# Kernel tuning notes

Hardware: AMD Instinct MI355X
Metric: run time of the kernel (lower is better)

The kernel has to match this reference:

```python
import jax, jax.numpy as jnp
import numpy as np

ALPHA = 0.2  # LeakyReLU negative slope


def setup_inputs() -> dict:
    key = jax.random.key(0)
    k1, k2, k3, k4 = jax.random.split(key, 4)
    B, Cin, Cout, N, T, Kt = 8, 64, 64, 2048, 13, 3
    L = T - Kt + 1  # 11, must equal `length`
    x = jax.random.normal(k1, (B, Cin, N, T), dtype=jnp.float32)
    w0 = jax.random.normal(k2, (Cout, Cin, 1, Kt), dtype=jnp.float32) * 0.05
    b0 = jax.random.normal(k3, (Cout,), dtype=jnp.float32) * 0.05
    w1 = jax.random.normal(k4, (Cout * L,), dtype=jnp.float32) * 0.05
    return {"x": x, "w0": w0, "b0": b0, "w1": w1}


def reference(x, w0, b0, w1):
    # conv0: Conv2d(in,out,(1,Kt)), VALID padding -> [B, Cout, N, L]
    h = jax.lax.conv_general_dilated(
        x, w0, window_strides=(1, 1), padding='VALID',
        dimension_numbers=('NCHW', 'OIHW', 'NCHW')) + b0[None, :, None, None]
    B, C, N, L = h.shape
    # permute(0,1,3,2).view(B, C*L, N) then 1x1 Conv1d (no bias) == contraction over (c,l)
    # NOTE: original module uses conv1 for BOTH f_1 and f_2 (conv2 unused), so f_1 == f_2.
    f = jnp.einsum('bcnl,cl->bn', h, w1.reshape(C, L))  # [B, N]
    logits = f[:, :, None] + f[:, None, :]              # [B, N, N]
    lrelu = jnp.where(logits >= 0, logits, ALPHA * logits)
    attention = jax.nn.softmax(lrelu, axis=-1)          # softmax over last (column) dim
    attention = jnp.swapaxes(attention, -1, -2)         # [B, N, N] transposed
    # h_prime[b,c,q,l] = sum_n h[b,c,n,l] * attention[b,n,q]
    h_prime = jnp.einsum('bcnl,bnq->bcql', h, attention)
    return h_prime, attention
```

## Files before the change

### kernel.cpp

```cpp
#include <hip/hip_runtime.h>

#define BB 8
#define CIN 64
#define COUT 64
#define NN 2048
#define TT 13
#define KTT 3
#define LL 11
#define CL 704
#define HP_SIZE 11534336LL

#define BM 176
#define BN 128
#define A_TILE 5632

#define WS_TAB_OFF 65568ULL
#define WS_W0PK_OFF 327712ULL
#define WS_APAN_OFF 352288ULL

typedef _Float16 f16;
typedef __attribute__((ext_vector_type(8))) _Float16 f16x8;
typedef __attribute__((ext_vector_type(2))) _Float16 f16x2;
typedef __attribute__((ext_vector_type(4))) float f32x4;

__device__ __forceinline__ unsigned int pk16(float a, float b) {
  f16 ha = (f16)a, hb = (f16)b;
  unsigned short ua = __builtin_bit_cast(unsigned short, ha);
  unsigned short ub = __builtin_bit_cast(unsigned short, hb);
  return (unsigned int)ua | ((unsigned int)ub << 16);
}
__device__ __forceinline__ f16x2 as_h2(unsigned int u) {
  return __builtin_bit_cast(f16x2, u);
}

__global__ __launch_bounds__(256) void k_pack(const float* __restrict__ w0,
                                              unsigned int* __restrict__ w0pk_g) {
  int tid = blockIdx.x * 256 + threadIdx.x;
  int c = tid & 63, r = tid >> 6;
  int kt = r % 3, cip = r / 3;
  float ev = w0[c * 192 + cip * 6 + kt];
  float od = w0[c * 192 + cip * 6 + 3 + kt];
  w0pk_g[r * 64 + c] = pk16(ev, od);
}

__global__ __launch_bounds__(512, 4) void k_conv(
    const float* __restrict__ x, const unsigned int* __restrict__ w0pk_g,
    const float* __restrict__ b0, const float* __restrict__ w1,
    f16* __restrict__ Apan, float* __restrict__ f) {
  __shared__ unsigned int w0pk[96 * 64];
  __shared__ unsigned int xspk[32 * 8 * 16];
  __shared__ f16 As[704 * 10];
  const int tid = threadIdx.x;
  const int b = blockIdx.x >> 8;
  const int n0 = (blockIdx.x & 255) << 3;

#pragma unroll
  for (int i = 0; i < 12; ++i) w0pk[i * 512 + tid] = w0pk_g[i * 512 + tid];

#pragma unroll
  for (int i = 0; i < 7; ++i) {
    int task = i * 512 + tid;
    if (task < 3328) {
      int cip = task / 104, rem = task - cip * 104;
      long long base = (long long)(b * 64 + 2 * cip) * 26624 + n0 * 13 + rem;
      float ev = x[base];
      float od = x[base + 26624];
      int n = rem / 13, t = rem - n * 13;
      xspk[(cip * 8 + n) * 16 + t] = pk16(ev, od);
    }
  }
  __syncthreads();

  const int c = tid & 63, w = tid >> 6;
  float acc[11];
  const float bias = b0[c];
#pragma unroll
  for (int l = 0; l < 11; ++l) acc[l] = bias;

  for (int cip = 0; cip < 32; ++cip) {
    const unsigned int* xr = &xspk[(cip * 8 + w) * 16];
    uint4 xa = *(const uint4*)xr;
    uint4 xb = *(const uint4*)(xr + 4);
    uint4 xc = *(const uint4*)(xr + 8);
    unsigned int x13[13] = {xa.x, xa.y, xa.z, xa.w, xb.x, xb.y, xb.z, xb.w,
                            xc.x, xc.y, xc.z, xc.w, xr[12]};
    f16x2 wk0 = as_h2(w0pk[(cip * 3 + 0) * 64 + c]);
    f16x2 wk1 = as_h2(w0pk[(cip * 3 + 1) * 64 + c]);
    f16x2 wk2 = as_h2(w0pk[(cip * 3 + 2) * 64 + c]);
#pragma unroll
    for (int l = 0; l < 11; ++l) {
      acc[l] = __builtin_amdgcn_fdot2(as_h2(x13[l]), wk0, acc[l], false);
      acc[l] = __builtin_amdgcn_fdot2(as_h2(x13[l + 1]), wk1, acc[l], false);
      acc[l] = __builtin_amdgcn_fdot2(as_h2(x13[l + 2]), wk2, acc[l], false);
    }
  }

  float p = 0.f;
#pragma unroll
  for (int l = 0; l < 11; ++l) p = fmaf(acc[l], w1[c * 11 + l], p);
#pragma unroll
  for (int off = 32; off; off >>= 1) p += __shfl_xor(p, off, 64);
  if (c == 0) f[b * 2048 + n0 + w] = p;

#pragma unroll
  for (int l = 0; l < 11; ++l) As[(c * 11 + l) * 10 + w] = (f16)acc[l];
  __syncthreads();

  const int ks = n0 >> 5, kc4 = (n0 >> 3) & 3;
  const unsigned int* As32 = (const unsigned int*)As;
#pragma unroll
  for (int i = 0; i < 2; ++i) {
    int m = i * 512 + tid;
    if (m < 704) {
      uint4 v;
      v.x = As32[m * 5 + 0];
      v.y = As32[m * 5 + 1];
      v.z = As32[m * 5 + 2];
      v.w = As32[m * 5 + 3];
      int ct = m / 176, mo = m - ct * 176;
      long long base = ((long long)(b * 4 + ct) * 64 + ks) * A_TILE + kc4 * 1408 + mo * 8;
      *(uint4*)&Apan[base] = v;
    }
  }
}

__global__ __launch_bounds__(256) void k_maxf(const float* __restrict__ f,
                                              float* __restrict__ maxf) {
  const int b = blockIdx.x, tid = threadIdx.x;
  float m = -1e30f;
  for (int i = tid; i < 2048; i += 256) m = fmaxf(m, f[b * 2048 + i]);
#pragma unroll
  for (int off = 32; off; off >>= 1) m = fmaxf(m, __shfl_xor(m, off, 64));
  __shared__ float red[4];
  if ((tid & 63) == 0) red[tid >> 6] = m;
  __syncthreads();
  if (tid == 0) maxf[b] = fmaxf(fmaxf(red[0], red[1]), fmaxf(red[2], red[3]));
}

__global__ __launch_bounds__(256) void k_rowsum(const float* __restrict__ f,
                                                const float* __restrict__ maxf,
                                                float4* __restrict__ tab4) {
  __shared__ float fs[2048];
  const int b = blockIdx.x >> 9;
  const int q0 = (blockIdx.x & 511) << 2;
  const int tid = threadIdx.x;
#pragma unroll
  for (int i = 0; i < 8; ++i) fs[i * 256 + tid] = f[b * 2048 + i * 256 + tid];
  __syncthreads();
  const int lane = tid & 63, wid = tid >> 6;
  const int q = q0 + wid;
  const float fq = fs[q];
  const float mb = maxf[b];
  float t = fq + mb;
  const float m = t >= 0.f ? t : 0.2f * t;
  float sum = 0.f;
  for (int j = lane; j < 2048; j += 64) {
    float v = fq + fs[j];
    v = v >= 0.f ? v : 0.2f * v;
    sum += __expf(v - m);
  }
#pragma unroll
  for (int off = 32; off; off >>= 1) sum += __shfl_xor(sum, off, 64);
  if (lane == 0) {
    float rq = 1.0f / sum;
    float En = __expf(fq - mb);
    float E2 = __expf(0.2f * fq);
    float Rq = t >= 0.f ? rq : rq * __expf(0.8f * t);
    float Sq = rq * __expf(0.2f * fq - m);
    tab4[b * 2048 + q] = make_float4(En, E2, Rq, Sq);
  }
}

__global__ __launch_bounds__(256, 2) void k_gemm(const f16* __restrict__ Apan,
                                                 const float* __restrict__ f,
                                                 const float4* __restrict__ tab4,
                                                 float* __restrict__ att,
                                                 float* __restrict__ out) {
  __shared__ __align__(16) f16 Abuf[2][A_TILE];
  __shared__ __align__(16) f16 Bbuf[2][4096];
  __shared__ float fs[2048];
  __shared__ __align__(16) float2 Etab[2048];

  const int p = blockIdx.x;
  const int g = (p & 7) | ((p >> 7) << 3);
  const int qt = (p >> 3) & 15;
  const int ct = g & 3, b = g >> 2;

  const int tid = threadIdx.x;
  const int w = tid >> 6, lane = tid & 63, qp = lane & 15, gg = lane >> 4;
  const int wq = w * 32;
  const f16* Ab = Apan + (long long)(b * 4 + ct) * 64 * A_TILE;
  const float* fb = f + b * NN;
  const float4* tb = tab4 + (long long)b * NN;

#pragma unroll
  for (int i = 0; i < 2; ++i)
    ((float4*)fs)[i * 256 + tid] = ((const float4*)fb)[i * 256 + tid];
#pragma unroll
  for (int i = 0; i < 8; ++i) {
    float4 v = tb[i * 256 + tid];
    Etab[i * 256 + tid] = make_float2(v.x, v.y);
  }

  const int qb = tid & 127, kh = tid >> 7;
  const float fq = fb[qt * 128 + qb];
  const float4 myt = tb[qt * 128 + qb];
  const float Rq = myt.z, Sq = myt.w;

  f32x4 acc[11][2];
#pragma unroll
  for (int mf = 0; mf < 11; ++mf)
#pragma unroll
    for (int nf = 0; nf < 2; ++nf) acc[mf][nf] = (f32x4){0.f, 0.f, 0.f, 0.f};

  auto stageA = [&](int ks, int bsel) {
    const f16* a = Ab + (long long)ks * A_TILE;
    f16* l = Abuf[bsel];
#pragma unroll
    for (int i = 0; i < 3; ++i) {
      int ch = i * 4 + w;
      if (ch < 11)
        __builtin_amdgcn_global_load_lds(
            (const __attribute__((address_space(1))) unsigned int*)(a + ch * 512 + lane * 8),
            (__attribute__((address_space(3))) unsigned int*)(l + ch * 512), 16, 0, 0);
    }
  };
  auto buildB = [&](int ks, int bsel) {
    f16* Bs = Bbuf[bsel];
    const int nbase = ks * 32 + kh * 16;
#pragma unroll
    for (int h8 = 0; h8 < 2; ++h8) {
      float4 fA = *(const float4*)&fs[nbase + h8 * 8];
      float4 fB = *(const float4*)&fs[nbase + h8 * 8 + 4];
      const float4* ep = (const float4*)&Etab[nbase + h8 * 8];
      float4 e0 = ep[0], e1 = ep[1], e2 = ep[2], e3 = ep[3];
      float fn[8] = {fA.x, fA.y, fA.z, fA.w, fB.x, fB.y, fB.z, fB.w};
      float Ev[8] = {e0.x, e0.z, e1.x, e1.z, e2.x, e2.z, e3.x, e3.z};
      float E2v[8] = {e0.y, e0.w, e1.y, e1.w, e2.y, e2.w, e3.y, e3.w};
      f16x8 v8;
      float vf[8];
#pragma unroll
      for (int u = 0; u < 8; ++u) {
        bool pos = (fq + fn[u]) >= 0.f;
        float val = (pos ? Ev[u] : E2v[u]) * (pos ? Rq : Sq);
        vf[u] = val;
        v8[u] = (f16)val;
      }
      *(f16x8*)&Bs[((kh * 2 + h8) * 128 + qb) * 8] = v8;
      if ((ks >> 4) == ct) {
        long long nb = (long long)(b * 2048 + nbase + h8 * 8) * 2048 + qt * 128 + qb;
#pragma unroll
        for (int u = 0; u < 8; ++u) att[nb + (long long)u * 2048] = vf[u];
      }
    }
  };
  auto compute = [&](int bsel) {
    const f16* A = Abuf[bsel];
    const f16* Bt = Bbuf[bsel];
    f16x8 bh[2];
#pragma unroll
    for (int nf = 0; nf < 2; ++nf)
      bh[nf] = *(const f16x8*)&Bt[(gg * 128 + wq + nf * 16 + qp) * 8];
#pragma unroll
    for (int mf = 0; mf < 11; ++mf) {
      f16x8 av = *(const f16x8*)&A[(gg * 176 + mf * 16 + qp) * 8];
#pragma unroll
      for (int nf = 0; nf < 2; ++nf)
        acc[mf][nf] = __builtin_amdgcn_mfma_f32_16x16x32_f16(av, bh[nf], acc[mf][nf], 0, 0, 0);
    }
  };

  stageA(0, 0);
  __syncthreads();
  buildB(0, 0);
  __syncthreads();

  int cur = 0;
  for (int ks = 0; ks < 63; ++ks) {
    stageA(ks + 1, cur ^ 1);
    buildB(ks + 1, cur ^ 1);
    compute(cur);
    __syncthreads();
    cur ^= 1;
  }
  compute(cur);

  float* ob = out + (long long)b * COUT * NN * LL;
#pragma unroll
  for (int mf = 0; mf < 11; ++mf) {
#pragma unroll
    for (int r = 0; r < 4; ++r) {
      int m = ct * BM + mf * 16 + gg * 4 + r;
      int c = m / 11, l2 = m - c * 11;
      float* orow = ob + (long long)c * NN * LL + l2;
#pragma unroll
      for (int nf = 0; nf < 2; ++nf) {
        int q = qt * BN + wq + nf * 16 + qp;
        orow[(long long)q * LL] = acc[mf][nf][r];
      }
    }
  }
}

extern "C" void kernel_launch(void* const* d_in, const int* in_sizes, int n_in,
                              void* d_out, int out_size, void* d_ws, size_t ws_size,
                              hipStream_t stream) {
  const float* x  = (const float*)d_in[0];
  const float* w0 = (const float*)d_in[1];
  const float* b0 = (const float*)d_in[2];
  const float* w1 = (const float*)d_in[3];

  float* fbuf = (float*)d_ws;
  float* maxf = fbuf + BB * NN;
  float4* tab4 = (float4*)((char*)d_ws + WS_TAB_OFF);
  unsigned int* w0pk_g = (unsigned int*)((char*)d_ws + WS_W0PK_OFF);
  f16* Apan = (f16*)((char*)d_ws + WS_APAN_OFF);

  float* hp  = (float*)d_out;
  float* att = hp + HP_SIZE;

  k_pack<<<dim3(24), dim3(256), 0, stream>>>(w0, w0pk_g);
  k_conv<<<dim3(BB * 256), dim3(512), 0, stream>>>(x, w0pk_g, b0, w1, Apan, fbuf);
  k_maxf<<<dim3(BB), dim3(256), 0, stream>>>(fbuf, maxf);
  k_rowsum<<<dim3(BB * 512), dim3(256), 0, stream>>>(fbuf, maxf, tab4);
  k_gemm<<<dim3(512), dim3(256), 0, stream>>>(Apan, fbuf, tab4, att, hp);
}
```

Baseline: 161.3 us.

## Split attention write into separate kernel and widen GEMM tile to 256 columns

Moves the fp32 attention-matrix store out of the GEMM's B-tile builder into a dedicated k_att kernel that writes rows with coalesced float4 stores, where before it was a strided per-element store. The GEMM now uses 512-thread blocks with a 176x256 tile, so each block builds B for twice as many columns and covers the 11 M-fragments with two wave groups. This removes the uncoalesced global writes from the GEMM's inner loop and halves the grid. In exchange it adds a launch, recomputes the attention values a second time, and leaves the second wave group with uneven fragment work.

```diff
diff --git a/kernel.cpp b/kernel.cpp
--- a/kernel.cpp
+++ b/kernel.cpp
@@ -11,7 +11,7 @@
 #define HP_SIZE 11534336LL
 
 #define BM 176
-#define BN 128
+#define BN 256
 #define A_TILE 5632
 
 #define WS_TAB_OFF 65568ULL
@@ -31,6 +31,11 @@
 }
 __device__ __forceinline__ f16x2 as_h2(unsigned int u) {
   return __builtin_bit_cast(f16x2, u);
+}
+__device__ __forceinline__ void gl_lds16(const f16* g, f16* l) {
+  __builtin_amdgcn_global_load_lds(
+      (const __attribute__((address_space(1))) unsigned int*)g,
+      (__attribute__((address_space(3))) unsigned int*)l, 16, 0, 0);
 }
 
 __global__ __launch_bounds__(256) void k_pack(const float* __restrict__ w0,
@@ -171,58 +176,95 @@
   }
 }
 
-__global__ __launch_bounds__(256, 2) void k_gemm(const f16* __restrict__ Apan,
+__global__ __launch_bounds__(256) void k_att(const float* __restrict__ f,
+                                             const float4* __restrict__ tab4,
+                                             float* __restrict__ att) {
+  const int b = blockIdx.x >> 9;
+  const int i0 = (blockIdx.x & 511) << 2;
+  const int tid = threadIdx.x;
+  const float* fb = f + b * NN;
+  const float4* tb = tab4 + (long long)b * NN;
+
+  float fi[4], En[4], E2[4];
+#pragma unroll
+  for (int r = 0; r < 4; ++r) {
+    fi[r] = fb[i0 + r];
+    float4 t = tb[i0 + r];
+    En[r] = t.x;
+    E2[r] = t.y;
+  }
+  const int j0 = tid * 8;
+  float4 fj0 = *(const float4*)&fb[j0];
+  float4 fj1 = *(const float4*)&fb[j0 + 4];
+  float fj[8] = {fj0.x, fj0.y, fj0.z, fj0.w, fj1.x, fj1.y, fj1.z, fj1.w};
+  float Rq[8], Sq[8];
+#pragma unroll
+  for (int u = 0; u < 8; ++u) {
+    float4 t = tb[j0 + u];
+    Rq[u] = t.z;
+    Sq[u] = t.w;
+  }
+  float* ab = att + ((long long)(b * 2048 + i0)) * 2048 + j0;
+#pragma unroll
+  for (int r = 0; r < 4; ++r) {
+    float o[8];
+#pragma unroll
+    for (int u = 0; u < 8; ++u) {
+      bool pos = (fi[r] + fj[u]) >= 0.f;
+      o[u] = (pos ? En[r] : E2[r]) * (pos ? Rq[u] : Sq[u]);
+    }
+    float* orow = ab + (long long)r * 2048;
+    *(float4*)&orow[0] = make_float4(o[0], o[1], o[2], o[3]);
+    *(float4*)&orow[4] = make_float4(o[4], o[5], o[6], o[7]);
+  }
+}
+
+__global__ __launch_bounds__(512, 2) void k_gemm(const f16* __restrict__ Apan,
                                                  const float* __restrict__ f,
                                                  const float4* __restrict__ tab4,
-                                                 float* __restrict__ att,
                                                  float* __restrict__ out) {
   __shared__ __align__(16) f16 Abuf[2][A_TILE];
-  __shared__ __align__(16) f16 Bbuf[2][4096];
+  __shared__ __align__(16) f16 Bbuf[2][8192];
   __shared__ float fs[2048];
   __shared__ __align__(16) float2 Etab[2048];
 
   const int p = blockIdx.x;
-  const int g = (p & 7) | ((p >> 7) << 3);
-  const int qt = (p >> 3) & 15;
+  const int g = (p & 7) | ((p >> 6) << 3);
+  const int qt = (p >> 3) & 7;
   const int ct = g & 3, b = g >> 2;
 
   const int tid = threadIdx.x;
   const int w = tid >> 6, lane = tid & 63, qp = lane & 15, gg = lane >> 4;
-  const int wq = w * 32;
+  const int qw = w & 3, mw = w >> 2;
   const f16* Ab = Apan + (long long)(b * 4 + ct) * 64 * A_TILE;
   const float* fb = f + b * NN;
   const float4* tb = tab4 + (long long)b * NN;
 
-#pragma unroll
-  for (int i = 0; i < 2; ++i)
-    ((float4*)fs)[i * 256 + tid] = ((const float4*)fb)[i * 256 + tid];
-#pragma unroll
-  for (int i = 0; i < 8; ++i) {
-    float4 v = tb[i * 256 + tid];
-    Etab[i * 256 + tid] = make_float2(v.x, v.y);
-  }
-
-  const int qb = tid & 127, kh = tid >> 7;
-  const float fq = fb[qt * 128 + qb];
-  const float4 myt = tb[qt * 128 + qb];
+  ((float4*)fs)[tid] = ((const float4*)fb)[tid];
+#pragma unroll
+  for (int i = 0; i < 4; ++i) {
+    float4 v = tb[i * 512 + tid];
+    Etab[i * 512 + tid] = make_float2(v.x, v.y);
+  }
+
+  const int qb = tid & 255, kh = tid >> 8;
+  const float fq = fb[qt * 256 + qb];
+  const float4 myt = tb[qt * 256 + qb];
   const float Rq = myt.z, Sq = myt.w;
 
-  f32x4 acc[11][2];
-#pragma unroll
-  for (int mf = 0; mf < 11; ++mf)
-#pragma unroll
-    for (int nf = 0; nf < 2; ++nf) acc[mf][nf] = (f32x4){0.f, 0.f, 0.f, 0.f};
+  f32x4 acc[6][4];
+#pragma unroll
+  for (int j = 0; j < 6; ++j)
+#pragma unroll
+    for (int nf = 0; nf < 4; ++nf) acc[j][nf] = (f32x4){0.f, 0.f, 0.f, 0.f};
 
   auto stageA = [&](int ks, int bsel) {
     const f16* a = Ab + (long long)ks * A_TILE;
     f16* l = Abuf[bsel];
 #pragma unroll
-    for (int i = 0; i < 3; ++i) {
-      int ch = i * 4 + w;
-      if (ch < 11)
-        __builtin_amdgcn_global_load_lds(
-            (const __attribute__((address_space(1))) unsigned int*)(a + ch * 512 + lane * 8),
-            (__attribute__((address_space(3))) unsigned int*)(l + ch * 512), 16, 0, 0);
+    for (int i = 0; i < 2; ++i) {
+      int ch = i * 8 + w;
+      if (ch < 11) gl_lds16(a + ch * 512 + lane * 8, l + ch * 512);
     }
   };
   auto buildB = [&](int ks, int bsel) {
@@ -238,35 +280,30 @@
       float Ev[8] = {e0.x, e0.z, e1.x, e1.z, e2.x, e2.z, e3.x, e3.z};
       float E2v[8] = {e0.y, e0.w, e1.y, e1.w, e2.y, e2.w, e3.y, e3.w};
       f16x8 v8;
-      float vf[8];
 #pragma unroll
       for (int u = 0; u < 8; ++u) {
         bool pos = (fq + fn[u]) >= 0.f;
-        float val = (pos ? Ev[u] : E2v[u]) * (pos ? Rq : Sq);
-        vf[u] = val;
-        v8[u] = (f16)val;
+        v8[u] = (f16)((pos ? Ev[u] : E2v[u]) * (pos ? Rq : Sq));
       }
-      *(f16x8*)&Bs[((kh * 2 + h8) * 128 + qb) * 8] = v8;
-      if ((ks >> 4) == ct) {
-        long long nb = (long long)(b * 2048 + nbase + h8 * 8) * 2048 + qt * 128 + qb;
-#pragma unroll
-        for (int u = 0; u < 8; ++u) att[nb + (long long)u * 2048] = vf[u];
-      }
+      *(f16x8*)&Bs[((kh * 2 + h8) * 256 + qb) * 8] = v8;
     }
   };
   auto compute = [&](int bsel) {
     const f16* A = Abuf[bsel];
     const f16* Bt = Bbuf[bsel];
-    f16x8 bh[2];
-#pragma unroll
-    for (int nf = 0; nf < 2; ++nf)
-      bh[nf] = *(const f16x8*)&Bt[(gg * 128 + wq + nf * 16 + qp) * 8];
-#pragma unroll
-    for (int mf = 0; mf < 11; ++mf) {
-      f16x8 av = *(const f16x8*)&A[(gg * 176 + mf * 16 + qp) * 8];
-#pragma unroll
-      for (int nf = 0; nf < 2; ++nf)
-        acc[mf][nf] = __builtin_amdgcn_mfma_f32_16x16x32_f16(av, bh[nf], acc[mf][nf], 0, 0, 0);
+    f16x8 bh[4];
+#pragma unroll
+    for (int nf = 0; nf < 4; ++nf)
+      bh[nf] = *(const f16x8*)&Bt[(gg * 256 + qw * 64 + nf * 16 + qp) * 8];
+#pragma unroll
+    for (int j = 0; j < 6; ++j) {
+      if (mw == 0 || j < 5) {
+        int mf = mw * 6 + j;
+        f16x8 av = *(const f16x8*)&A[(gg * 176 + mf * 16 + qp) * 8];
+#pragma unroll
+        for (int nf = 0; nf < 4; ++nf)
+          acc[j][nf] = __builtin_amdgcn_mfma_f32_16x16x32_f16(av, bh[nf], acc[j][nf], 0, 0, 0);
+      }
     }
   };
 
@@ -287,16 +324,19 @@
 
   float* ob = out + (long long)b * COUT * NN * LL;
 #pragma unroll
-  for (int mf = 0; mf < 11; ++mf) {
-#pragma unroll
-    for (int r = 0; r < 4; ++r) {
-      int m = ct * BM + mf * 16 + gg * 4 + r;
-      int c = m / 11, l2 = m - c * 11;
-      float* orow = ob + (long long)c * NN * LL + l2;
-#pragma unroll
-      for (int nf = 0; nf < 2; ++nf) {
-        int q = qt * BN + wq + nf * 16 + qp;
-        orow[(long long)q * LL] = acc[mf][nf][r];
+  for (int j = 0; j < 6; ++j) {
+    if (mw == 0 || j < 5) {
+      int mf = mw * 6 + j;
+#pragma unroll
+      for (int r = 0; r < 4; ++r) {
+        int m = ct * BM + mf * 16 + gg * 4 + r;
+        int c = m / 11, l2 = m - c * 11;
+        float* orow = ob + (long long)c * NN * LL + l2;
+#pragma unroll
+        for (int nf = 0; nf < 4; ++nf) {
+          int q = qt * BN + qw * 64 + nf * 16 + qp;
+          orow[(long long)q * LL] = acc[j][nf][r];
+        }
       }
     }
   }
@@ -323,5 +363,6 @@
   k_conv<<<dim3(BB * 256), dim3(512), 0, stream>>>(x, w0pk_g, b0, w1, Apan, fbuf);
   k_maxf<<<dim3(BB), dim3(256), 0, stream>>>(fbuf, maxf);
   k_rowsum<<<dim3(BB * 512), dim3(256), 0, stream>>>(fbuf, maxf, tab4);
-  k_gemm<<<dim3(512), dim3(256), 0, stream>>>(Apan, fbuf, tab4, att, hp);
-}
+  k_att<<<dim3(BB * 512), dim3(256), 0, stream>>>(fbuf, tab4, att);
+  k_gemm<<<dim3(256), dim3(512), 0, stream>>>(Apan, fbuf, tab4, hp);
+}
```

After: 185.2 us. +14.8%, slower.

## Enlarge GEMM M-tile to 352 with 32x32 MFMA and 512-thread blocks

Applied to the files above, without the earlier changes.

Restructures the attention-weighted GEMM so each block covers 352 rows of the (c,l) dimension with 8 waves, switching from 16x16x32 to 32x32x16 MFMA and changing the A-panel layout written by the conv kernel to match. It also replaces the LeakyReLU sign test on fq+fn with a comparison of a precomputed exponential against a per-row threshold, which removes the shared f array. Compute is now issued before building the next B tile. The aim is more reuse of each B tile and half as many blocks rebuilding B, at the cost of higher register use and uneven M work per wave (3 vs 2 subtiles).

```diff
diff --git a/kernel.cpp b/kernel.cpp
--- a/kernel.cpp
+++ b/kernel.cpp
@@ -10,9 +10,9 @@
 #define CL 704
 #define HP_SIZE 11534336LL
 
-#define BM 176
+#define BM 352
 #define BN 128
-#define A_TILE 5632
+#define A_TILE 11264
 
 #define WS_TAB_OFF 65568ULL
 #define WS_W0PK_OFF 327712ULL
@@ -21,7 +21,7 @@
 typedef _Float16 f16;
 typedef __attribute__((ext_vector_type(8))) _Float16 f16x8;
 typedef __attribute__((ext_vector_type(2))) _Float16 f16x2;
-typedef __attribute__((ext_vector_type(4))) float f32x4;
+typedef __attribute__((ext_vector_type(16))) float f32x16;
 
 __device__ __forceinline__ unsigned int pk16(float a, float b) {
   f16 ha = (f16)a, hb = (f16)b;
@@ -31,6 +31,11 @@
 }
 __device__ __forceinline__ f16x2 as_h2(unsigned int u) {
   return __builtin_bit_cast(f16x2, u);
+}
+__device__ __forceinline__ void gl_lds16(const f16* g, f16* l) {
+  __builtin_amdgcn_global_load_lds(
+      (const __attribute__((address_space(1))) unsigned int*)g,
+      (__attribute__((address_space(3))) unsigned int*)l, 16, 0, 0);
 }
 
 __global__ __launch_bounds__(256) void k_pack(const float* __restrict__ w0,
@@ -106,7 +111,7 @@
   for (int l = 0; l < 11; ++l) As[(c * 11 + l) * 10 + w] = (f16)acc[l];
   __syncthreads();
 
-  const int ks = n0 >> 5, kc4 = (n0 >> 3) & 3;
+  const int ks = n0 >> 5, kc = (n0 >> 4) & 1, kh = (n0 >> 3) & 1;
   const unsigned int* As32 = (const unsigned int*)As;
 #pragma unroll
   for (int i = 0; i < 2; ++i) {
@@ -117,8 +122,10 @@
       v.y = As32[m * 5 + 1];
       v.z = As32[m * 5 + 2];
       v.w = As32[m * 5 + 3];
-      int ct = m / 176, mo = m - ct * 176;
-      long long base = ((long long)(b * 4 + ct) * 64 + ks) * A_TILE + kc4 * 1408 + mo * 8;
+      int ct = m / 352, mr = m - ct * 352;
+      int msub = mr >> 5, row = m & 31;
+      long long base = (long long)((b * 2 + ct) * 64 + ks) * A_TILE +
+                       kc * 5632 + msub * 512 + kh * 256 + row * 8;
       *(uint4*)&Apan[base] = v;
     }
   }
@@ -171,102 +178,99 @@
   }
 }
 
-__global__ __launch_bounds__(256, 2) void k_gemm(const f16* __restrict__ Apan,
+__global__ __launch_bounds__(512, 2) void k_gemm(const f16* __restrict__ Apan,
                                                  const float* __restrict__ f,
+                                                 const float* __restrict__ maxf,
                                                  const float4* __restrict__ tab4,
                                                  float* __restrict__ att,
                                                  float* __restrict__ out) {
   __shared__ __align__(16) f16 Abuf[2][A_TILE];
   __shared__ __align__(16) f16 Bbuf[2][4096];
-  __shared__ float fs[2048];
   __shared__ __align__(16) float2 Etab[2048];
 
   const int p = blockIdx.x;
-  const int g = (p & 7) | ((p >> 7) << 3);
-  const int qt = (p >> 3) & 15;
-  const int ct = g & 3, b = g >> 2;
+  const int g = p & 15, qt = p >> 4;
+  const int ct = g & 1, b = g >> 1;
 
   const int tid = threadIdx.x;
-  const int w = tid >> 6, lane = tid & 63, qp = lane & 15, gg = lane >> 4;
-  const int wq = w * 32;
-  const f16* Ab = Apan + (long long)(b * 4 + ct) * 64 * A_TILE;
-  const float* fb = f + b * NN;
+  const int w = tid >> 6, lane = tid & 63;
+  const int qw = w & 1, mw = w >> 1;
+  const int l31 = lane & 31, l5 = lane >> 5;
+  const int nsub = (mw < 3) ? 3 : 2;
+
+  const f16* Ab = Apan + (long long)((b * 2 + ct) * 64) * A_TILE;
   const float4* tb = tab4 + (long long)b * NN;
 
 #pragma unroll
-  for (int i = 0; i < 2; ++i)
-    ((float4*)fs)[i * 256 + tid] = ((const float4*)fb)[i * 256 + tid];
-#pragma unroll
-  for (int i = 0; i < 8; ++i) {
-    float4 v = tb[i * 256 + tid];
-    Etab[i * 256 + tid] = make_float2(v.x, v.y);
-  }
-
-  const int qb = tid & 127, kh = tid >> 7;
-  const float fq = fb[qt * 128 + qb];
-  const float4 myt = tb[qt * 128 + qb];
-  const float Rq = myt.z, Sq = myt.w;
-
-  f32x4 acc[11][2];
-#pragma unroll
-  for (int mf = 0; mf < 11; ++mf)
-#pragma unroll
-    for (int nf = 0; nf < 2; ++nf) acc[mf][nf] = (f32x4){0.f, 0.f, 0.f, 0.f};
+  for (int i = 0; i < 4; ++i) {
+    int idx = i * 512 + tid;
+    float4 v = tb[idx];
+    Etab[idx] = make_float2(v.x, v.y);
+  }
+
+  const int qb = tid & 127, kg = tid >> 7;
+  const float fq = f[b * NN + qt * 128 + qb];
+  const float4 qt4 = tb[qt * 128 + qb];
+  const float Rq = qt4.z, Sq = qt4.w;
+  const float thrE = __expf(-fq - maxf[b]);
+
+  f32x16 acc[3][2];
+#pragma unroll
+  for (int j = 0; j < 3; ++j)
+#pragma unroll
+    for (int nf = 0; nf < 2; ++nf)
+#pragma unroll
+      for (int z = 0; z < 16; ++z) acc[j][nf][z] = 0.f;
 
   auto stageA = [&](int ks, int bsel) {
     const f16* a = Ab + (long long)ks * A_TILE;
     f16* l = Abuf[bsel];
 #pragma unroll
     for (int i = 0; i < 3; ++i) {
-      int ch = i * 4 + w;
-      if (ch < 11)
-        __builtin_amdgcn_global_load_lds(
-            (const __attribute__((address_space(1))) unsigned int*)(a + ch * 512 + lane * 8),
-            (__attribute__((address_space(3))) unsigned int*)(l + ch * 512), 16, 0, 0);
+      int ch = i * 512 + tid;
+      if (ch < 1408) gl_lds16(a + ch * 8, l + ch * 8);
     }
   };
-  auto buildB = [&](int ks, int bsel) {
-    f16* Bs = Bbuf[bsel];
-    const int nbase = ks * 32 + kh * 16;
-#pragma unroll
-    for (int h8 = 0; h8 < 2; ++h8) {
-      float4 fA = *(const float4*)&fs[nbase + h8 * 8];
-      float4 fB = *(const float4*)&fs[nbase + h8 * 8 + 4];
-      const float4* ep = (const float4*)&Etab[nbase + h8 * 8];
-      float4 e0 = ep[0], e1 = ep[1], e2 = ep[2], e3 = ep[3];
-      float fn[8] = {fA.x, fA.y, fA.z, fA.w, fB.x, fB.y, fB.z, fB.w};
-      float Ev[8] = {e0.x, e0.z, e1.x, e1.z, e2.x, e2.z, e3.x, e3.z};
-      float E2v[8] = {e0.y, e0.w, e1.y, e1.w, e2.y, e2.w, e3.y, e3.w};
-      f16x8 v8;
-      float vf[8];
-#pragma unroll
-      for (int u = 0; u < 8; ++u) {
-        bool pos = (fq + fn[u]) >= 0.f;
-        float val = (pos ? Ev[u] : E2v[u]) * (pos ? Rq : Sq);
-        vf[u] = val;
-        v8[u] = (f16)val;
-      }
-      *(f16x8*)&Bs[((kh * 2 + h8) * 128 + qb) * 8] = v8;
-      if ((ks >> 4) == ct) {
-        long long nb = (long long)(b * 2048 + nbase + h8 * 8) * 2048 + qt * 128 + qb;
-#pragma unroll
-        for (int u = 0; u < 8; ++u) att[nb + (long long)u * 2048] = vf[u];
-      }
+  auto buildB = [&](int ksn, int bsel) {
+    const float4* ep = (const float4*)&Etab[ksn * 32 + kg * 8];
+    float4 e0 = ep[0], e1 = ep[1], e2 = ep[2], e3 = ep[3];
+    float En[8] = {e0.x, e0.z, e1.x, e1.z, e2.x, e2.z, e3.x, e3.z};
+    float E2[8] = {e0.y, e0.w, e1.y, e1.w, e2.y, e2.w, e3.y, e3.w};
+    f16x8 v8;
+    float vf[8];
+#pragma unroll
+    for (int u = 0; u < 8; ++u) {
+      bool pos = En[u] >= thrE;
+      float val = (pos ? En[u] : E2[u]) * (pos ? Rq : Sq);
+      vf[u] = val;
+      v8[u] = (f16)val;
+    }
+    *(f16x8*)&Bbuf[bsel][kg * 1024 + qb * 8] = v8;
+    if ((ksn >> 5) == ct) {
+      long long nb = (long long)(b * 2048 + ksn * 32 + kg * 8) * 2048 + qt * 128 + qb;
+#pragma unroll
+      for (int u = 0; u < 8; ++u) att[nb + (long long)u * 2048] = vf[u];
     }
   };
   auto compute = [&](int bsel) {
     const f16* A = Abuf[bsel];
     const f16* Bt = Bbuf[bsel];
-    f16x8 bh[2];
-#pragma unroll
-    for (int nf = 0; nf < 2; ++nf)
-      bh[nf] = *(const f16x8*)&Bt[(gg * 128 + wq + nf * 16 + qp) * 8];
-#pragma unroll
-    for (int mf = 0; mf < 11; ++mf) {
-      f16x8 av = *(const f16x8*)&A[(gg * 176 + mf * 16 + qp) * 8];
+#pragma unroll
+    for (int kc = 0; kc < 2; ++kc) {
+      f16x8 bv[2];
 #pragma unroll
       for (int nf = 0; nf < 2; ++nf)
-        acc[mf][nf] = __builtin_amdgcn_mfma_f32_16x16x32_f16(av, bh[nf], acc[mf][nf], 0, 0, 0);
+        bv[nf] = *(const f16x8*)&Bt[kc * 2048 + l5 * 1024 + (qw * 64 + nf * 32 + l31) * 8];
+#pragma unroll
+      for (int j = 0; j < 3; ++j) {
+        if (j < nsub) {
+          int ms = mw * 3 + j;
+          f16x8 av = *(const f16x8*)&A[kc * 5632 + ms * 512 + l5 * 256 + l31 * 8];
+#pragma unroll
+          for (int nf = 0; nf < 2; ++nf)
+            acc[j][nf] = __builtin_amdgcn_mfma_f32_32x32x16_f16(av, bv[nf], acc[j][nf], 0, 0, 0);
+        }
+      }
     }
   };
 
@@ -278,8 +282,8 @@
   int cur = 0;
   for (int ks = 0; ks < 63; ++ks) {
     stageA(ks + 1, cur ^ 1);
+    compute(cur);
     buildB(ks + 1, cur ^ 1);
-    compute(cur);
     __syncthreads();
     cur ^= 1;
   }
@@ -287,16 +291,21 @@
 
   float* ob = out + (long long)b * COUT * NN * LL;
 #pragma unroll
-  for (int mf = 0; mf < 11; ++mf) {
-#pragma unroll
-    for (int r = 0; r < 4; ++r) {
-      int m = ct * BM + mf * 16 + gg * 4 + r;
-      int c = m / 11, l2 = m - c * 11;
-      float* orow = ob + (long long)c * NN * LL + l2;
-#pragma unroll
-      for (int nf = 0; nf < 2; ++nf) {
-        int q = qt * BN + wq + nf * 16 + qp;
-        orow[(long long)q * LL] = acc[mf][nf][r];
+  for (int j = 0; j < 3; ++j) {
+    if (j < nsub) {
+#pragma unroll
+      for (int rq = 0; rq < 4; ++rq) {
+#pragma unroll
+        for (int r = 0; r < 4; ++r) {
+          int row = r + rq * 8 + l5 * 4;
+          int m = ct * BM + (mw * 3 + j) * 32 + row;
+          int c = m / 11, l2 = m - c * 11;
+#pragma unroll
+          for (int nf = 0; nf < 2; ++nf) {
+            int q = qt * BN + qw * 64 + nf * 32 + l31;
+            ob[((long long)c * NN + q) * LL + l2] = acc[j][nf][rq * 4 + r];
+          }
+        }
       }
     }
   }
@@ -323,5 +332,5 @@
   k_conv<<<dim3(BB * 256), dim3(512), 0, stream>>>(x, w0pk_g, b0, w1, Apan, fbuf);
   k_maxf<<<dim3(BB), dim3(256), 0, stream>>>(fbuf, maxf);
   k_rowsum<<<dim3(BB * 512), dim3(256), 0, stream>>>(fbuf, maxf, tab4);
-  k_gemm<<<dim3(512), dim3(256), 0, stream>>>(Apan, fbuf, tab4, att, hp);
-}
+  k_gemm<<<dim3(256), dim3(512), 0, stream>>>(Apan, fbuf, maxf, tab4, att, hp);
+}
```

Measured after the change: 173.6 us. +7.7%, slower.

## Retile attention GEMM to 64x256 tiles with register-fed A operands

Applied to the files above, without the earlier changes.

The A panel layout is changed so each block owns a 64-row M tile (11 tiles per batch) and 256 query columns, giving 704 blocks. A fragments now come straight from global memory into registers with one-step prefetch, replacing the double-buffered LDS staging. The B operand is built per wave directly in registers, so there is no shared B buffer and no per-step barrier. The leaky-relu branch select becomes a max of the two exponential terms, which removes the f-value table from shared memory. Each block's B values are recomputed more often across M tiles, and att ownership is now split by an ks*11>>6 mapping.

```diff
diff --git a/kernel.cpp b/kernel.cpp
--- a/kernel.cpp
+++ b/kernel.cpp
@@ -9,10 +9,6 @@
 #define LL 11
 #define CL 704
 #define HP_SIZE 11534336LL
-
-#define BM 176
-#define BN 128
-#define A_TILE 5632
 
 #define WS_TAB_OFF 65568ULL
 #define WS_W0PK_OFF 327712ULL
@@ -106,7 +102,7 @@
   for (int l = 0; l < 11; ++l) As[(c * 11 + l) * 10 + w] = (f16)acc[l];
   __syncthreads();
 
-  const int ks = n0 >> 5, kc4 = (n0 >> 3) & 3;
+  const int ks = n0 >> 5, kgrp = (n0 >> 3) & 3;
   const unsigned int* As32 = (const unsigned int*)As;
 #pragma unroll
   for (int i = 0; i < 2; ++i) {
@@ -117,8 +113,9 @@
       v.y = As32[m * 5 + 1];
       v.z = As32[m * 5 + 2];
       v.w = As32[m * 5 + 3];
-      int ct = m / 176, mo = m - ct * 176;
-      long long base = ((long long)(b * 4 + ct) * 64 + ks) * A_TILE + kc4 * 1408 + mo * 8;
+      int mt = m >> 6, fr = (m >> 4) & 3, r16 = m & 15;
+      long long base = ((long long)(b * 11 + mt) * 64 + ks) * 2048 +
+                       fr * 512 + (kgrp * 16 + r16) * 8;
       *(uint4*)&Apan[base] = v;
     }
   }
@@ -171,132 +168,102 @@
   }
 }
 
-__global__ __launch_bounds__(256, 2) void k_gemm(const f16* __restrict__ Apan,
-                                                 const float* __restrict__ f,
+__global__ __launch_bounds__(256, 3) void k_gemm(const f16* __restrict__ Apan,
                                                  const float4* __restrict__ tab4,
                                                  float* __restrict__ att,
                                                  float* __restrict__ out) {
-  __shared__ __align__(16) f16 Abuf[2][A_TILE];
-  __shared__ __align__(16) f16 Bbuf[2][4096];
-  __shared__ float fs[2048];
   __shared__ __align__(16) float2 Etab[2048];
 
   const int p = blockIdx.x;
-  const int g = (p & 7) | ((p >> 7) << 3);
-  const int qt = (p >> 3) & 15;
-  const int ct = g & 3, b = g >> 2;
+  const int g = p % 88, qt = p / 88;
+  const int b = g / 11, mt = g % 11;
 
   const int tid = threadIdx.x;
-  const int w = tid >> 6, lane = tid & 63, qp = lane & 15, gg = lane >> 4;
-  const int wq = w * 32;
-  const f16* Ab = Apan + (long long)(b * 4 + ct) * 64 * A_TILE;
-  const float* fb = f + b * NN;
+  const int qw = tid >> 6, lane = tid & 63;
+  const int l15 = lane & 15, l4 = lane >> 4;
+
+  const f16* Ab = Apan + ((long long)(b * 11 + mt) * 64) * 2048 + lane * 8;
   const float4* tb = tab4 + (long long)b * NN;
 
 #pragma unroll
-  for (int i = 0; i < 2; ++i)
-    ((float4*)fs)[i * 256 + tid] = ((const float4*)fb)[i * 256 + tid];
-#pragma unroll
   for (int i = 0; i < 8; ++i) {
-    float4 v = tb[i * 256 + tid];
-    Etab[i * 256 + tid] = make_float2(v.x, v.y);
-  }
-
-  const int qb = tid & 127, kh = tid >> 7;
-  const float fq = fb[qt * 128 + qb];
-  const float4 myt = tb[qt * 128 + qb];
-  const float Rq = myt.z, Sq = myt.w;
-
-  f32x4 acc[11][2];
-#pragma unroll
-  for (int mf = 0; mf < 11; ++mf)
-#pragma unroll
-    for (int nf = 0; nf < 2; ++nf) acc[mf][nf] = (f32x4){0.f, 0.f, 0.f, 0.f};
-
-  auto stageA = [&](int ks, int bsel) {
-    const f16* a = Ab + (long long)ks * A_TILE;
-    f16* l = Abuf[bsel];
-#pragma unroll
-    for (int i = 0; i < 3; ++i) {
-      int ch = i * 4 + w;
-      if (ch < 11)
-        __builtin_amdgcn_global_load_lds(
-            (const __attribute__((address_space(1))) unsigned int*)(a + ch * 512 + lane * 8),
-            (__attribute__((address_space(3))) unsigned int*)(l + ch * 512), 16, 0, 0);
-    }
-  };
-  auto buildB = [&](int ks, int bsel) {
-    f16* Bs = Bbuf[bsel];
-    const int nbase = ks * 32 + kh * 16;
-#pragma unroll
-    for (int h8 = 0; h8 < 2; ++h8) {
-      float4 fA = *(const float4*)&fs[nbase + h8 * 8];
-      float4 fB = *(const float4*)&fs[nbase + h8 * 8 + 4];
-      const float4* ep = (const float4*)&Etab[nbase + h8 * 8];
-      float4 e0 = ep[0], e1 = ep[1], e2 = ep[2], e3 = ep[3];
-      float fn[8] = {fA.x, fA.y, fA.z, fA.w, fB.x, fB.y, fB.z, fB.w};
-      float Ev[8] = {e0.x, e0.z, e1.x, e1.z, e2.x, e2.z, e3.x, e3.z};
-      float E2v[8] = {e0.y, e0.w, e1.y, e1.w, e2.y, e2.w, e3.y, e3.w};
-      f16x8 v8;
+    int idx = i * 256 + tid;
+    float4 v = tb[idx];
+    Etab[idx] = make_float2(v.x, v.y);
+  }
+  const int q0 = qt * 256 + qw * 64 + l15;
+  float Rq0, Sq0, Rq1, Sq1, Rq2, Sq2, Rq3, Sq3;
+  { float4 t4 = tb[q0];      Rq0 = t4.z; Sq0 = t4.w; }
+  { float4 t4 = tb[q0 + 16]; Rq1 = t4.z; Sq1 = t4.w; }
+  { float4 t4 = tb[q0 + 32]; Rq2 = t4.z; Sq2 = t4.w; }
+  { float4 t4 = tb[q0 + 48]; Rq3 = t4.z; Sq3 = t4.w; }
+  __syncthreads();
+
+  f32x4 acc[4][4];
+#pragma unroll
+  for (int fr = 0; fr < 4; ++fr)
+#pragma unroll
+    for (int nf = 0; nf < 4; ++nf) acc[fr][nf] = (f32x4){0.f, 0.f, 0.f, 0.f};
+
+  f16x8 c0 = *(const f16x8*)(Ab);
+  f16x8 c1 = *(const f16x8*)(Ab + 512);
+  f16x8 c2 = *(const f16x8*)(Ab + 1024);
+  f16x8 c3 = *(const f16x8*)(Ab + 1536);
+
+  for (int ks = 0; ks < 64; ++ks) {
+    f16x8 n0 = c0, n1 = c1, n2 = c2, n3 = c3;
+    if (ks < 63) {
+      const f16* at = Ab + (ks + 1) * 2048;
+      n0 = *(const f16x8*)(at);
+      n1 = *(const f16x8*)(at + 512);
+      n2 = *(const f16x8*)(at + 1024);
+      n3 = *(const f16x8*)(at + 1536);
+    }
+    const int nb = ks * 32 + l4 * 8;
+    const float4* ep = (const float4*)&Etab[nb];
+    float4 e0 = ep[0], e1 = ep[1], e2 = ep[2], e3 = ep[3];
+    float En[8] = {e0.x, e0.z, e1.x, e1.z, e2.x, e2.z, e3.x, e3.z};
+    float E2[8] = {e0.y, e0.w, e1.y, e1.w, e2.y, e2.w, e3.y, e3.w};
+    const bool owned = ((ks * 11) >> 6) == mt;
+    const long long abase = ((long long)(b * 2048 + nb)) * 2048 + q0;
+
+#pragma unroll
+    for (int nf = 0; nf < 4; ++nf) {
+      const float Rq = nf == 0 ? Rq0 : nf == 1 ? Rq1 : nf == 2 ? Rq2 : Rq3;
+      const float Sq = nf == 0 ? Sq0 : nf == 1 ? Sq1 : nf == 2 ? Sq2 : Sq3;
+      f16x8 bv;
       float vf[8];
 #pragma unroll
       for (int u = 0; u < 8; ++u) {
-        bool pos = (fq + fn[u]) >= 0.f;
-        float val = (pos ? Ev[u] : E2v[u]) * (pos ? Rq : Sq);
+        float val = fmaxf(En[u] * Rq, E2[u] * Sq);
         vf[u] = val;
-        v8[u] = (f16)val;
+        bv[u] = (f16)val;
       }
-      *(f16x8*)&Bs[((kh * 2 + h8) * 128 + qb) * 8] = v8;
-      if ((ks >> 4) == ct) {
-        long long nb = (long long)(b * 2048 + nbase + h8 * 8) * 2048 + qt * 128 + qb;
-#pragma unroll
-        for (int u = 0; u < 8; ++u) att[nb + (long long)u * 2048] = vf[u];
+      if (owned) {
+        float* ap = att + abase + nf * 16;
+#pragma unroll
+        for (int u = 0; u < 8; ++u) ap[(long long)u * 2048] = vf[u];
       }
-    }
-  };
-  auto compute = [&](int bsel) {
-    const f16* A = Abuf[bsel];
-    const f16* Bt = Bbuf[bsel];
-    f16x8 bh[2];
-#pragma unroll
-    for (int nf = 0; nf < 2; ++nf)
-      bh[nf] = *(const f16x8*)&Bt[(gg * 128 + wq + nf * 16 + qp) * 8];
-#pragma unroll
-    for (int mf = 0; mf < 11; ++mf) {
-      f16x8 av = *(const f16x8*)&A[(gg * 176 + mf * 16 + qp) * 8];
-#pragma unroll
-      for (int nf = 0; nf < 2; ++nf)
-        acc[mf][nf] = __builtin_amdgcn_mfma_f32_16x16x32_f16(av, bh[nf], acc[mf][nf], 0, 0, 0);
-    }
-  };
-
-  stageA(0, 0);
-  __syncthreads();
-  buildB(0, 0);
-  __syncthreads();
-
-  int cur = 0;
-  for (int ks = 0; ks < 63; ++ks) {
-    stageA(ks + 1, cur ^ 1);
-    buildB(ks + 1, cur ^ 1);
-    compute(cur);
-    __syncthreads();
-    cur ^= 1;
-  }
-  compute(cur);
+      acc[0][nf] = __builtin_amdgcn_mfma_f32_16x16x32_f16(c0, bv, acc[0][nf], 0, 0, 0);
+      acc[1][nf] = __builtin_amdgcn_mfma_f32_16x16x32_f16(c1, bv, acc[1][nf], 0, 0, 0);
+      acc[2][nf] = __builtin_amdgcn_mfma_f32_16x16x32_f16(c2, bv, acc[2][nf], 0, 0, 0);
+      acc[3][nf] = __builtin_amdgcn_mfma_f32_16x16x32_f16(c3, bv, acc[3][nf], 0, 0, 0);
+    }
+    c0 = n0; c1 = n1; c2 = n2; c3 = n3;
+  }
 
   float* ob = out + (long long)b * COUT * NN * LL;
 #pragma unroll
-  for (int mf = 0; mf < 11; ++mf) {
+  for (int fr = 0; fr < 4; ++fr) {
 #pragma unroll
     for (int r = 0; r < 4; ++r) {
-      int m = ct * BM + mf * 16 + gg * 4 + r;
+      int m = mt * 64 + fr * 16 + l4 * 4 + r;
       int c = m / 11, l2 = m - c * 11;
       float* orow = ob + (long long)c * NN * LL + l2;
 #pragma unroll
-      for (int nf = 0; nf < 2; ++nf) {
-        int q = qt * BN + wq + nf * 16 + qp;
-        orow[(long long)q * LL] = acc[mf][nf][r];
+      for (int nf = 0; nf < 4; ++nf) {
+        int q = q0 + nf * 16;
+        orow[(long long)q * LL] = acc[fr][nf][r];
       }
     }
   }
@@ -323,5 +290,5 @@
   k_conv<<<dim3(BB * 256), dim3(512), 0, stream>>>(x, w0pk_g, b0, w1, Apan, fbuf);
   k_maxf<<<dim3(BB), dim3(256), 0, stream>>>(fbuf, maxf);
   k_rowsum<<<dim3(BB * 512), dim3(256), 0, stream>>>(fbuf, maxf, tab4);
-  k_gemm<<<dim3(512), dim3(256), 0, stream>>>(Apan, fbuf, tab4, att, hp);
-}
+  k_gemm<<<dim3(704), dim3(256), 0, stream>>>(Apan, tab4, att, hp);
+}
```

New measurement: 158.7 us. No clear change (-1.6%).
